# Performance work log

Measured on AMD Instinct MI355X. Metric: run time of the kernel, lower is better.

Reference implementation:

```python
import math
import jax, jax.numpy as jnp
import numpy as np

D_MODEL = 1024
NUM_HEADS = 16
HEAD_DIM = D_MODEL // NUM_HEADS
MAX_REL = 128


def setup_inputs() -> dict:
    key = jax.random.key(0)
    ks = jax.random.split(key, 7)
    B, S = 2, 2048
    s = 1.0 / math.sqrt(D_MODEL)
    return {
        "x": jax.random.normal(ks[0], (B, S, D_MODEL), dtype=jnp.float32),
        "mask": jnp.ones((B, S, S), dtype=jnp.int32),
        "w_q": jax.random.normal(ks[1], (D_MODEL, D_MODEL), dtype=jnp.float32) * s,
        "w_k": jax.random.normal(ks[2], (D_MODEL, D_MODEL), dtype=jnp.float32) * s,
        "w_v": jax.random.normal(ks[3], (D_MODEL, D_MODEL), dtype=jnp.float32) * s,
        "w_o_w": jax.random.normal(ks[4], (D_MODEL, D_MODEL), dtype=jnp.float32) * s,
        "w_o_b": jnp.zeros((D_MODEL,), dtype=jnp.float32),
        "rel_emb": jax.random.normal(ks[5], (2 * MAX_REL + 1, HEAD_DIM), dtype=jnp.float32),
    }


def reference(x, mask, w_q, w_k, w_v, w_o_w, w_o_b, rel_emb):
    B, S, D = x.shape
    H, hd = NUM_HEADS, HEAD_DIM
    scale = math.sqrt(hd)

    def proj(w):  # torch Linear: x @ w.T  -> [B,H,S,hd]
        return (x @ w.T).reshape(B, S, H, hd).transpose(0, 2, 1, 3)

    Q, K, V = proj(w_q), proj(w_k), proj(w_v)

    # content scores (scaled)
    scores = jnp.einsum("bhqd,bhkd->bhqk", Q, K) / scale

    # T5-style relative position bias (NOT scaled, matching source)
    pos = jnp.arange(S)
    dist = jnp.clip(pos[None, :] - pos[:, None], -MAX_REL, MAX_REL) + MAX_REL  # [S,S]
    rel = rel_emb[dist]  # [S,S,hd]
    scores = scores + jnp.einsum("bhqd,qkd->bhqk", Q, rel)

    scores = jnp.where(mask[:, None, :, :] == 0, -1e9, scores)
    attn = jax.nn.softmax(scores, axis=-1)  # [B,H,S,S]

    ctx = jnp.einsum("bhqk,bhkd->bhqd", attn, V)
    ctx = ctx.transpose(0, 2, 1, 3).reshape(B, S, D)
    out = ctx @ w_o_w.T + w_o_b
    return out, attn
```

## Files before the change

### kernel.cpp

```cpp
#include <hip/hip_runtime.h>
#include <hip/hip_bf16.h>

#define B_ 2
#define S_ 2048
#define H_ 16
#define HD_ 64
#define D_ 1024
#define NJ_ 257
#define RSTRIDE_ 264

typedef __bf16 v8bf __attribute__((ext_vector_type(8)));
typedef __bf16 v4bf __attribute__((ext_vector_type(4)));
typedef float  v4f  __attribute__((ext_vector_type(4)));

static __device__ __forceinline__ v4f mfma16(v8bf a, v8bf b, v4f c) {
    return __builtin_amdgcn_mfma_f32_16x16x32_bf16(a, b, c, 0, 0, 0);
}

__global__ void k_split2(const float* __restrict__ src, __bf16* __restrict__ h,
                         __bf16* __restrict__ l, int n4) {
    int i = blockIdx.x * blockDim.x + threadIdx.x;
    int stride = gridDim.x * blockDim.x;
    for (; i < n4; i += stride) {
        const float4 v = ((const float4*)src)[i];
        float vv[4] = {v.x, v.y, v.z, v.w};
        v4bf hv, lv;
#pragma unroll
        for (int j = 0; j < 4; j++) {
            __bf16 hb = (__bf16)vv[j];
            hv[j] = hb;
            lv[j] = (__bf16)(vv[j] - (float)hb);
        }
        *(v4bf*)(h + 4 * (size_t)i) = hv;
        *(v4bf*)(l + 4 * (size_t)i) = lv;
    }
}

__global__ void k_rowflag(const int* __restrict__ mask, unsigned char* __restrict__ flags) {
    const int row = blockIdx.x;
    const int4* mp = (const int4*)(mask + (size_t)row * S_);
    int ok = 1;
    for (int i = threadIdx.x; i < S_ / 4; i += blockDim.x) {
        int4 m = mp[i];
        ok &= (m.x != 0) & (m.y != 0) & (m.z != 0) & (m.w != 0);
    }
    int all = __syncthreads_and(ok);
    if (threadIdx.x == 0) flags[row] = (unsigned char)(all != 0);
}

__global__ __launch_bounds__(256) void k_proj(const __bf16* __restrict__ Ah,
                                              const __bf16* __restrict__ Al,
                                              const __bf16* __restrict__ Bh,
                                              const __bf16* __restrict__ Bl,
                                              __bf16* __restrict__ Oh,
                                              __bf16* __restrict__ Ol) {
    __shared__ __bf16 sAh[64][72], sAl[64][72], sBh[64][72], sBl[64][72];
    const int n0 = blockIdx.x * 64;
    const int m0 = blockIdx.y * 64;
    const int tid = threadIdx.x, lane = tid & 63, wid = tid >> 6;
    const int fr = lane & 15, fo = (lane >> 4) * 8;
    const int srow = tid >> 2, scol = (tid & 3) * 16;
    v4f acc[4] = {};
    for (int k0 = 0; k0 < D_; k0 += 64) {
        const size_t ga = (size_t)(m0 + srow) * D_ + k0 + scol;
        const size_t gb = (size_t)(n0 + srow) * D_ + k0 + scol;
        *(v8bf*)&sAh[srow][scol]     = *(const v8bf*)(Ah + ga);
        *(v8bf*)&sAh[srow][scol + 8] = *(const v8bf*)(Ah + ga + 8);
        *(v8bf*)&sAl[srow][scol]     = *(const v8bf*)(Al + ga);
        *(v8bf*)&sAl[srow][scol + 8] = *(const v8bf*)(Al + ga + 8);
        *(v8bf*)&sBh[srow][scol]     = *(const v8bf*)(Bh + gb);
        *(v8bf*)&sBh[srow][scol + 8] = *(const v8bf*)(Bh + gb + 8);
        *(v8bf*)&sBl[srow][scol]     = *(const v8bf*)(Bl + gb);
        *(v8bf*)&sBl[srow][scol + 8] = *(const v8bf*)(Bl + gb + 8);
        __syncthreads();
#pragma unroll
        for (int ks = 0; ks < 2; ks++) {
            v8bf ah = *(const v8bf*)&sAh[wid * 16 + fr][ks * 32 + fo];
            v8bf al = *(const v8bf*)&sAl[wid * 16 + fr][ks * 32 + fo];
#pragma unroll
            for (int nt = 0; nt < 4; nt++) {
                v8bf bh = *(const v8bf*)&sBh[nt * 16 + fr][ks * 32 + fo];
                v8bf bl = *(const v8bf*)&sBl[nt * 16 + fr][ks * 32 + fo];
                acc[nt] = mfma16(ah, bh, acc[nt]);
                acc[nt] = mfma16(ah, bl, acc[nt]);
                acc[nt] = mfma16(al, bh, acc[nt]);
            }
        }
        __syncthreads();
    }
#pragma unroll
    for (int nt = 0; nt < 4; nt++) {
#pragma unroll
        for (int r = 0; r < 4; r++) {
            const int row = m0 + wid * 16 + (lane >> 4) * 4 + r;
            const int col = n0 + nt * 16 + fr;
            const size_t idx = (size_t)row * D_ + col;
            float f = acc[nt][r];
            __bf16 hb = (__bf16)f;
            Oh[idx] = hb;
            Ol[idx] = (__bf16)(f - (float)hb);
        }
    }
}

__global__ __launch_bounds__(256) void k_projV(const __bf16* __restrict__ A,
                                               const __bf16* __restrict__ Bw,
                                               __bf16* __restrict__ O) {
    __shared__ __bf16 sA[64][72], sB[64][72];
    const int n0 = blockIdx.x * 64;
    const int m0 = blockIdx.y * 64;
    const int tid = threadIdx.x, lane = tid & 63, wid = tid >> 6;
    const int fr = lane & 15, fo = (lane >> 4) * 8;
    const int srow = tid >> 2, scol = (tid & 3) * 16;
    v4f acc[4] = {};
    for (int k0 = 0; k0 < D_; k0 += 64) {
        const size_t ga = (size_t)(m0 + srow) * D_ + k0 + scol;
        const size_t gb = (size_t)(n0 + srow) * D_ + k0 + scol;
        *(v8bf*)&sA[srow][scol]     = *(const v8bf*)(A + ga);
        *(v8bf*)&sA[srow][scol + 8] = *(const v8bf*)(A + ga + 8);
        *(v8bf*)&sB[srow][scol]     = *(const v8bf*)(Bw + gb);
        *(v8bf*)&sB[srow][scol + 8] = *(const v8bf*)(Bw + gb + 8);
        __syncthreads();
#pragma unroll
        for (int ks = 0; ks < 2; ks++) {
            v8bf a = *(const v8bf*)&sA[wid * 16 + fr][ks * 32 + fo];
#pragma unroll
            for (int nt = 0; nt < 4; nt++) {
                v8bf bb = *(const v8bf*)&sB[nt * 16 + fr][ks * 32 + fo];
                acc[nt] = mfma16(a, bb, acc[nt]);
            }
        }
        __syncthreads();
    }
#pragma unroll
    for (int nt = 0; nt < 4; nt++) {
#pragma unroll
        for (int r = 0; r < 4; r++) {
            const int row = m0 + wid * 16 + (lane >> 4) * 4 + r;
            O[(size_t)row * D_ + n0 + nt * 16 + fr] = (__bf16)acc[nt][r];
        }
    }
}

__global__ __launch_bounds__(256) void k_vtrans(const __bf16* __restrict__ Vb,
                                                __bf16* __restrict__ Vt) {
    __shared__ __bf16 t[64][72];
    const int s0 = blockIdx.x * 64, n0 = blockIdx.y * 64, b = blockIdx.z;
    const int tid = threadIdx.x;
    const int r = tid >> 2, c = (tid & 3) * 16;
    const size_t gin = ((size_t)(b * S_ + s0 + r)) * D_ + n0 + c;
    *(v8bf*)&t[r][c]     = *(const v8bf*)(Vb + gin);
    *(v8bf*)&t[r][c + 8] = *(const v8bf*)(Vb + gin + 8);
    __syncthreads();
    v8bf o0, o1;
#pragma unroll
    for (int j = 0; j < 8; j++) { o0[j] = t[c + j][r]; o1[j] = t[c + 8 + j][r]; }
    const size_t gout = ((size_t)(b * D_ + n0 + r)) * S_ + s0 + c;
    *(v8bf*)(Vt + gout)     = o0;
    *(v8bf*)(Vt + gout + 8) = o1;
}

__global__ __launch_bounds__(256) void k_relgemm(const __bf16* __restrict__ Qh,
                                                 const __bf16* __restrict__ Ql,
                                                 const __bf16* __restrict__ relh,
                                                 const __bf16* __restrict__ rell,
                                                 float* __restrict__ Rg) {
    const int q0 = blockIdx.x * 64;
    const int bh = blockIdx.y;
    const int b = bh >> 4, h = bh & 15;
    const int tid = threadIdx.x, lane = tid & 63, wid = tid >> 6;
    const int fr = lane & 15, fo = (lane >> 4) * 8;
    const size_t qbase = (size_t)(b * S_ + q0 + wid * 16 + fr) * D_ + h * HD_;
    v8bf qa_h[2], qa_l[2];
#pragma unroll
    for (int ks = 0; ks < 2; ks++) {
        qa_h[ks] = *(const v8bf*)(Qh + qbase + ks * 32 + fo);
        qa_l[ks] = *(const v8bf*)(Ql + qbase + ks * 32 + fo);
    }
    v4f acc[17] = {};
#pragma unroll
    for (int jt = 0; jt < 17; jt++) {
        int j = jt * 16 + fr;
        if (j > 256) j = 256;
        const size_t rb = (size_t)j * HD_;
#pragma unroll
        for (int ks = 0; ks < 2; ks++) {
            v8bf bh_ = *(const v8bf*)(relh + rb + ks * 32 + fo);
            v8bf bl_ = *(const v8bf*)(rell + rb + ks * 32 + fo);
            acc[jt] = mfma16(qa_h[ks], bh_, acc[jt]);
            acc[jt] = mfma16(qa_h[ks], bl_, acc[jt]);
            acc[jt] = mfma16(qa_l[ks], bh_, acc[jt]);
        }
    }
    const size_t rowbase = ((size_t)bh * S_ + q0 + wid * 16 + (lane >> 4) * 4) * RSTRIDE_;
#pragma unroll
    for (int jt = 0; jt < 17; jt++) {
        const int j = jt * 16 + fr;
        if (j <= 256) {
#pragma unroll
            for (int r = 0; r < 4; r++)
                Rg[rowbase + (size_t)r * RSTRIDE_ + j] = acc[jt][r];
        }
    }
}

__global__ __launch_bounds__(512, 4) void k_stats(const __bf16* __restrict__ Qh,
                                                  const __bf16* __restrict__ Ql,
                                                  const __bf16* __restrict__ Kh,
                                                  const float* __restrict__ Rg,
                                                  const int* __restrict__ mask,
                                                  const unsigned char* __restrict__ flags,
                                                  float* __restrict__ mrow,
                                                  float* __restrict__ lrow) {
    __shared__ __bf16 sK[2][64][72];
    const int flat = blockIdx.x;
    const int swz = (flat & 7) * 64 + (flat >> 3);
    const int qt = swz & 15, bh = swz >> 4;
    const int b = bh >> 4, h = bh & 15;
    const int q0 = qt * 128;
    const int tid = threadIdx.x, lane = tid & 63, w = tid >> 6;
    const int fr = lane & 15, fq = lane >> 4, fo = fq * 8;
    const int myrow = w * 16 + fq * 4;
    const int srow = tid >> 3, sc8 = (tid & 7) * 8;

    const size_t qbase = (size_t)(b * S_ + q0 + w * 16 + fr) * D_ + h * HD_;
    v8bf qa_h[2], qa_l[2];
#pragma unroll
    for (int ks = 0; ks < 2; ks++) {
        qa_h[ks] = *(const v8bf*)(Qh + qbase + ks * 32 + fo);
        qa_l[ks] = *(const v8bf*)(Ql + qbase + ks * 32 + fo);
    }

    const int qg0 = q0 + myrow;
    const size_t rbase0 = ((size_t)bh * S_ + qg0) * RSTRIDE_;
    const size_t mbase0 = ((size_t)b * S_ + qg0) * S_;
    float rcL[4], rcR[4];
    int flr[4];
#pragma unroll
    for (int r = 0; r < 4; r++) {
        rcL[r] = Rg[rbase0 + (size_t)r * RSTRIDE_];
        rcR[r] = Rg[rbase0 + (size_t)r * RSTRIDE_ + 256];
        flr[r] = flags[(size_t)b * S_ + qg0 + r];
    }

    const __bf16* kgbase = Kh + (size_t)(b * S_ + srow) * D_ + h * HD_ + sc8;
    v8bf rk = *(const v8bf*)(kgbase);
    *(v8bf*)&sK[0][srow][sc8] = rk;
    rk = *(const v8bf*)(kgbase + (size_t)64 * D_);
    __syncthreads();

    float mrun[4], lrun[4];
#pragma unroll
    for (int r = 0; r < 4; r++) { mrun[r] = -3.0e38f; lrun[r] = 0.0f; }

    int cur = 0;
    for (int kc = 0; kc < 32; kc++) {
        const int k0 = kc * 64;
        v4f acc[4] = {};
#pragma unroll
        for (int ct = 0; ct < 4; ct++) {
#pragma unroll
            for (int ks = 0; ks < 2; ks++) {
                v8bf kb = *(const v8bf*)&sK[cur][ct * 16 + fr][ks * 32 + fo];
                acc[ct] = mfma16(qa_h[ks], kb, acc[ct]);
                acc[ct] = mfma16(qa_l[ks], kb, acc[ct]);
            }
        }
        const bool band = (kc >= 2 * qt - 3) && (kc <= 2 * qt + 3);
        const bool left = kc < 2 * qt;
#pragma unroll
        for (int r = 0; r < 4; r++) {
            const int qg = qg0 + r;
            float s[4];
#pragma unroll
            for (int ct = 0; ct < 4; ct++) {
                const int k = k0 + ct * 16 + fr;
                float bias;
                if (band) {
                    const int dd = k - qg;
                    const int j = dd < -128 ? 0 : (dd > 128 ? 256 : dd + 128);
                    bias = Rg[rbase0 + (size_t)r * RSTRIDE_ + j];
                } else {
                    bias = left ? rcL[r] : rcR[r];
                }
                float sv = acc[ct][r] * 0.125f + bias;
                if (!flr[r] && mask[mbase0 + (size_t)r * S_ + k] == 0) sv = -1e9f;
                s[ct] = sv;
            }
            const float cm = fmaxf(fmaxf(s[0], s[1]), fmaxf(s[2], s[3]));
            if (cm > mrun[r]) {
                lrun[r] *= __expf(mrun[r] - cm);
                mrun[r] = cm;
            }
            lrun[r] += __expf(s[0] - mrun[r]) + __expf(s[1] - mrun[r]) +
                       __expf(s[2] - mrun[r]) + __expf(s[3] - mrun[r]);
        }
        if (kc < 31) *(v8bf*)&sK[cur ^ 1][srow][sc8] = rk;
        if (kc < 30) rk = *(const v8bf*)(kgbase + (size_t)(k0 + 128) * D_);
        __syncthreads();
        cur ^= 1;
    }

#pragma unroll
    for (int r = 0; r < 4; r++) {
#pragma unroll
        for (int sh = 1; sh < 16; sh <<= 1) {
            const float om = __shfl_xor(mrun[r], sh);
            const float ol = __shfl_xor(lrun[r], sh);
            const float mn = fmaxf(mrun[r], om);
            lrun[r] = lrun[r] * __expf(mrun[r] - mn) + ol * __expf(om - mn);
            mrun[r] = mn;
        }
    }
    if (fr == 0) {
#pragma unroll
        for (int r = 0; r < 4; r++) {
            mrow[(size_t)bh * S_ + qg0 + r] = mrun[r];
            lrow[(size_t)bh * S_ + qg0 + r] = lrun[r];
        }
    }
}

__global__ __launch_bounds__(512, 4) void k_final(const __bf16* __restrict__ Qh,
                                                  const __bf16* __restrict__ Ql,
                                                  const __bf16* __restrict__ Kh,
                                                  const __bf16* __restrict__ Vt,
                                                  const float* __restrict__ Rg,
                                                  const int* __restrict__ mask,
                                                  const unsigned char* __restrict__ flags,
                                                  const float* __restrict__ mrow,
                                                  const float* __restrict__ lrow,
                                                  float* __restrict__ attn,
                                                  __bf16* __restrict__ ctx) {
    __shared__ __bf16 sK[2][64][72], sV[2][64][72], sP[128][72];
    const int flat = blockIdx.x;
    const int swz = (flat & 7) * 64 + (flat >> 3);
    const int qt = swz & 15, bh = swz >> 4;
    const int b = bh >> 4, h = bh & 15;
    const int q0 = qt * 128;
    const int tid = threadIdx.x, lane = tid & 63, w = tid >> 6;
    const int fr = lane & 15, fq = lane >> 4, fo = fq * 8;
    const int myrow = w * 16 + fq * 4;
    const int srow = tid >> 3, sc8 = (tid & 7) * 8;

    const size_t qbase = (size_t)(b * S_ + q0 + w * 16 + fr) * D_ + h * HD_;
    v8bf qa_h[2], qa_l[2];
#pragma unroll
    for (int ks = 0; ks < 2; ks++) {
        qa_h[ks] = *(const v8bf*)(Qh + qbase + ks * 32 + fo);
        qa_l[ks] = *(const v8bf*)(Ql + qbase + ks * 32 + fo);
    }

    const int qg0 = q0 + myrow;
    const size_t rbase0 = ((size_t)bh * S_ + qg0) * RSTRIDE_;
    const size_t mbase0 = ((size_t)b * S_ + qg0) * S_;
    const size_t abase0 = ((size_t)bh * S_ + qg0) * S_;
    float rcL[4], rcR[4], mfin[4], lfin[4];
    int flr[4];
#pragma unroll
    for (int r = 0; r < 4; r++) {
        rcL[r] = Rg[rbase0 + (size_t)r * RSTRIDE_];
        rcR[r] = Rg[rbase0 + (size_t)r * RSTRIDE_ + 256];
        flr[r] = flags[(size_t)b * S_ + qg0 + r];
        mfin[r] = mrow[(size_t)bh * S_ + qg0 + r];
        lfin[r] = 1.0f / lrow[(size_t)bh * S_ + qg0 + r];
    }

    const __bf16* kgbase = Kh + (size_t)(b * S_ + srow) * D_ + h * HD_ + sc8;
    const __bf16* vgbase = Vt + (size_t)(b * D_ + h * HD_ + srow) * S_ + sc8;
    v8bf rk = *(const v8bf*)(kgbase);
    v8bf rv = *(const v8bf*)(vgbase);
    *(v8bf*)&sK[0][srow][sc8] = rk;
    *(v8bf*)&sV[0][srow][sc8] = rv;
    rk = *(const v8bf*)(kgbase + (size_t)64 * D_);
    rv = *(const v8bf*)(vgbase + 64);
    __syncthreads();

    v4f acc2[4] = {};
    int cur = 0;
    for (int kc = 0; kc < 32; kc++) {
        const int k0 = kc * 64;
        v4f acc[4] = {};
#pragma unroll
        for (int ct = 0; ct < 4; ct++) {
#pragma unroll
            for (int ks = 0; ks < 2; ks++) {
                v8bf kb = *(const v8bf*)&sK[cur][ct * 16 + fr][ks * 32 + fo];
                acc[ct] = mfma16(qa_h[ks], kb, acc[ct]);
                acc[ct] = mfma16(qa_l[ks], kb, acc[ct]);
            }
        }
        const bool band = (kc >= 2 * qt - 3) && (kc <= 2 * qt + 3);
        const bool left = kc < 2 * qt;
#pragma unroll
        for (int r = 0; r < 4; r++) {
            const int qg = qg0 + r;
#pragma unroll
            for (int ct = 0; ct < 4; ct++) {
                const int k = k0 + ct * 16 + fr;
                float bias;
                if (band) {
                    const int dd = k - qg;
                    const int j = dd < -128 ? 0 : (dd > 128 ? 256 : dd + 128);
                    bias = Rg[rbase0 + (size_t)r * RSTRIDE_ + j];
                } else {
                    bias = left ? rcL[r] : rcR[r];
                }
                float sv = acc[ct][r] * 0.125f + bias;
                if (!flr[r] && mask[mbase0 + (size_t)r * S_ + k] == 0) sv = -1e9f;
                const float p = __expf(sv - mfin[r]) * lfin[r];
                attn[abase0 + (size_t)r * S_ + k] = p;
                sP[myrow + r][ct * 16 + fr] = (__bf16)p;
            }
        }
        __syncthreads();
#pragma unroll
        for (int ks = 0; ks < 2; ks++) {
            v8bf pa = *(const v8bf*)&sP[w * 16 + fr][ks * 32 + fo];
#pragma unroll
            for (int ct = 0; ct < 4; ct++) {
                v8bf vb = *(const v8bf*)&sV[cur][ct * 16 + fr][ks * 32 + fo];
                acc2[ct] = mfma16(pa, vb, acc2[ct]);
            }
        }
        if (kc < 31) {
            *(v8bf*)&sK[cur ^ 1][srow][sc8] = rk;
            *(v8bf*)&sV[cur ^ 1][srow][sc8] = rv;
        }
        if (kc < 30) {
            rk = *(const v8bf*)(kgbase + (size_t)(k0 + 128) * D_);
            rv = *(const v8bf*)(vgbase + k0 + 128);
        }
        __syncthreads();
        cur ^= 1;
    }

#pragma unroll
    for (int ct = 0; ct < 4; ct++) {
#pragma unroll
        for (int r = 0; r < 4; r++) {
            const int qg = qg0 + r;
            const int d = ct * 16 + fr;
            ctx[(size_t)(b * S_ + qg) * D_ + h * HD_ + d] = (__bf16)acc2[ct][r];
        }
    }
}

__global__ __launch_bounds__(256) void k_outproj(const __bf16* __restrict__ A,
                                                 const __bf16* __restrict__ Bw,
                                                 const float* __restrict__ bias,
                                                 float* __restrict__ out) {
    __shared__ __bf16 sA[64][72], sB[64][72];
    const int n0 = blockIdx.x * 64;
    const int m0 = blockIdx.y * 64;
    const int tid = threadIdx.x, lane = tid & 63, wid = tid >> 6;
    const int fr = lane & 15, fo = (lane >> 4) * 8;
    const int srow = tid >> 2, scol = (tid & 3) * 16;
    v4f acc[4] = {};
    for (int k0 = 0; k0 < D_; k0 += 64) {
        const size_t ga = (size_t)(m0 + srow) * D_ + k0 + scol;
        const size_t gb = (size_t)(n0 + srow) * D_ + k0 + scol;
        *(v8bf*)&sA[srow][scol]     = *(const v8bf*)(A + ga);
        *(v8bf*)&sA[srow][scol + 8] = *(const v8bf*)(A + ga + 8);
        *(v8bf*)&sB[srow][scol]     = *(const v8bf*)(Bw + gb);
        *(v8bf*)&sB[srow][scol + 8] = *(const v8bf*)(Bw + gb + 8);
        __syncthreads();
#pragma unroll
        for (int ks = 0; ks < 2; ks++) {
            v8bf a = *(const v8bf*)&sA[wid * 16 + fr][ks * 32 + fo];
#pragma unroll
            for (int nt = 0; nt < 4; nt++) {
                v8bf bb = *(const v8bf*)&sB[nt * 16 + fr][ks * 32 + fo];
                acc[nt] = mfma16(a, bb, acc[nt]);
            }
        }
        __syncthreads();
    }
#pragma unroll
    for (int nt = 0; nt < 4; nt++) {
        const float bv = bias[n0 + nt * 16 + fr];
#pragma unroll
        for (int r = 0; r < 4; r++) {
            const int row = m0 + wid * 16 + (lane >> 4) * 4 + r;
            out[(size_t)row * D_ + n0 + nt * 16 + fr] = acc[nt][r] + bv;
        }
    }
}

extern "C" void kernel_launch(void* const* d_in, const int* in_sizes, int n_in,
                              void* d_out, int out_size, void* d_ws, size_t ws_size,
                              hipStream_t stream) {
    (void)in_sizes; (void)n_in; (void)out_size; (void)ws_size;
    const float* x    = (const float*)d_in[0];
    const int*   mask = (const int*)d_in[1];
    const float* wq   = (const float*)d_in[2];
    const float* wk   = (const float*)d_in[3];
    const float* wv   = (const float*)d_in[4];
    const float* wo   = (const float*)d_in[5];
    const float* wob  = (const float*)d_in[6];
    const float* rel  = (const float*)d_in[7];
    float* out  = (float*)d_out;
    float* attn = out + (size_t)B_ * S_ * D_;

    char* p = (char*)d_ws;
    auto alloc = [&](size_t bytes) -> char* {
        char* r = p;
        p += (bytes + 255) & ~(size_t)255;
        return r;
    };
    const size_t BSD = (size_t)B_ * S_ * D_;
    const size_t DD  = (size_t)D_ * D_;
    __bf16* xh   = (__bf16*)alloc(BSD * 2);
    __bf16* xl   = (__bf16*)alloc(BSD * 2);
    __bf16* wqh  = (__bf16*)alloc(DD * 2);
    __bf16* wql  = (__bf16*)alloc(DD * 2);
    __bf16* wkh  = (__bf16*)alloc(DD * 2);
    __bf16* wkl  = (__bf16*)alloc(DD * 2);
    __bf16* wvh  = (__bf16*)alloc(DD * 2);
    __bf16* wvl  = (__bf16*)alloc(DD * 2);
    __bf16* woh  = (__bf16*)alloc(DD * 2);
    __bf16* wol  = (__bf16*)alloc(DD * 2);
    __bf16* relh = (__bf16*)alloc((size_t)NJ_ * HD_ * 2);
    __bf16* rell = (__bf16*)alloc((size_t)NJ_ * HD_ * 2);
    __bf16* Qh   = (__bf16*)alloc(BSD * 2);
    __bf16* Ql   = (__bf16*)alloc(BSD * 2);
    __bf16* Kh   = (__bf16*)alloc(BSD * 2);
    __bf16* Kl   = (__bf16*)alloc(BSD * 2);
    __bf16* Vb   = (__bf16*)alloc(BSD * 2);
    __bf16* Vt   = (__bf16*)alloc(BSD * 2);
    float*  Rg   = (float*)alloc((size_t)B_ * H_ * S_ * RSTRIDE_ * 4);
    float*  mrow = (float*)alloc((size_t)B_ * H_ * S_ * 4);
    float*  lrow = (float*)alloc((size_t)B_ * H_ * S_ * 4);
    __bf16* ctx  = (__bf16*)alloc(BSD * 2);
    unsigned char* flags = (unsigned char*)alloc((size_t)B_ * S_);

    k_split2<<<2048, 256, 0, stream>>>(x, xh, xl, (int)(BSD / 4));
    k_split2<<<1024, 256, 0, stream>>>(wq, wqh, wql, (int)(DD / 4));
    k_split2<<<1024, 256, 0, stream>>>(wk, wkh, wkl, (int)(DD / 4));
    k_split2<<<1024, 256, 0, stream>>>(wv, wvh, wvl, (int)(DD / 4));
    k_split2<<<1024, 256, 0, stream>>>(wo, woh, wol, (int)(DD / 4));
    k_split2<<<17, 256, 0, stream>>>(rel, relh, rell, (int)(NJ_ * HD_ / 4));

    k_rowflag<<<B_ * S_, 256, 0, stream>>>(mask, flags);

    k_proj<<<dim3(D_ / 64, B_ * S_ / 64), 256, 0, stream>>>(xh, xl, wqh, wql, Qh, Ql);
    k_proj<<<dim3(D_ / 64, B_ * S_ / 64), 256, 0, stream>>>(xh, xl, wkh, wkl, Kh, Kl);
    k_projV<<<dim3(D_ / 64, B_ * S_ / 64), 256, 0, stream>>>(xh, wvh, Vb);

    k_vtrans<<<dim3(S_ / 64, D_ / 64, B_), 256, 0, stream>>>(Vb, Vt);

    k_relgemm<<<dim3(S_ / 64, B_ * H_), 256, 0, stream>>>(Qh, Ql, relh, rell, Rg);

    k_stats<<<512, 512, 0, stream>>>(Qh, Ql, Kh, Rg, mask, flags, mrow, lrow);

    k_final<<<512, 512, 0, stream>>>(Qh, Ql, Kh, Vt, Rg, mask, flags, mrow, lrow, attn, ctx);

    k_outproj<<<dim3(D_ / 64, B_ * S_ / 64), 256, 0, stream>>>(ctx, woh, wob, out);
}
```

Before: 608.9 us.

## Fuse stats and final attention passes into one kernel with direct global K/V reads

Merges the row-statistics kernel and the final probability/context kernel into one kernel that runs two passes over K per block, so the mrow/lrow intermediates and one launch are no longer needed. It also drops the shared-memory double-buffered K/V staging and block-wide barriers. Each wave now reads K and V fragments straight from global memory and keeps its P tile in a per-wave shared slice. This removes synchronisation and LDS traffic but relies on cache for K/V reuse across the 8 waves, which may raise global memory traffic and load latency.

```diff
diff --git a/kernel.cpp b/kernel.cpp
--- a/kernel.cpp
+++ b/kernel.cpp
@@ -204,15 +204,16 @@
     }
 }
 
-__global__ __launch_bounds__(512, 4) void k_stats(const __bf16* __restrict__ Qh,
+__global__ __launch_bounds__(512, 4) void k_attn2(const __bf16* __restrict__ Qh,
                                                   const __bf16* __restrict__ Ql,
                                                   const __bf16* __restrict__ Kh,
+                                                  const __bf16* __restrict__ Vt,
                                                   const float* __restrict__ Rg,
                                                   const int* __restrict__ mask,
                                                   const unsigned char* __restrict__ flags,
-                                                  float* __restrict__ mrow,
-                                                  float* __restrict__ lrow) {
-    __shared__ __bf16 sK[2][64][72];
+                                                  float* __restrict__ attn,
+                                                  __bf16* __restrict__ ctx) {
+    __shared__ __bf16 sP[8][16][72];
     const int flat = blockIdx.x;
     const int swz = (flat & 7) * 64 + (flat >> 3);
     const int qt = swz & 15, bh = swz >> 4;
@@ -220,8 +221,7 @@
     const int q0 = qt * 128;
     const int tid = threadIdx.x, lane = tid & 63, w = tid >> 6;
     const int fr = lane & 15, fq = lane >> 4, fo = fq * 8;
-    const int myrow = w * 16 + fq * 4;
-    const int srow = tid >> 3, sc8 = (tid & 7) * 8;
+    const int qg0 = q0 + w * 16 + fq * 4;
 
     const size_t qbase = (size_t)(b * S_ + q0 + w * 16 + fr) * D_ + h * HD_;
     v8bf qa_h[2], qa_l[2];
@@ -231,9 +231,9 @@
         qa_l[ks] = *(const v8bf*)(Ql + qbase + ks * 32 + fo);
     }
 
-    const int qg0 = q0 + myrow;
     const size_t rbase0 = ((size_t)bh * S_ + qg0) * RSTRIDE_;
     const size_t mbase0 = ((size_t)b * S_ + qg0) * S_;
+    const size_t abase0 = ((size_t)bh * S_ + qg0) * S_;
     float rcL[4], rcR[4];
     int flr[4];
 #pragma unroll
@@ -243,28 +243,25 @@
         flr[r] = flags[(size_t)b * S_ + qg0 + r];
     }
 
-    const __bf16* kgbase = Kh + (size_t)(b * S_ + srow) * D_ + h * HD_ + sc8;
-    v8bf rk = *(const v8bf*)(kgbase);
-    *(v8bf*)&sK[0][srow][sc8] = rk;
-    rk = *(const v8bf*)(kgbase + (size_t)64 * D_);
-    __syncthreads();
+    const __bf16* kpanel = Kh + (size_t)b * S_ * D_ + h * HD_;
+    const __bf16* vpanel = Vt + (size_t)(b * D_ + h * HD_) * S_;
 
     float mrun[4], lrun[4];
 #pragma unroll
     for (int r = 0; r < 4; r++) { mrun[r] = -3.0e38f; lrun[r] = 0.0f; }
 
-    int cur = 0;
     for (int kc = 0; kc < 32; kc++) {
         const int k0 = kc * 64;
         v4f acc[4] = {};
 #pragma unroll
         for (int ct = 0; ct < 4; ct++) {
-#pragma unroll
-            for (int ks = 0; ks < 2; ks++) {
-                v8bf kb = *(const v8bf*)&sK[cur][ct * 16 + fr][ks * 32 + fo];
-                acc[ct] = mfma16(qa_h[ks], kb, acc[ct]);
-                acc[ct] = mfma16(qa_l[ks], kb, acc[ct]);
-            }
+            const size_t krow = (size_t)(k0 + ct * 16 + fr) * D_;
+            v8bf kb0 = *(const v8bf*)(kpanel + krow + fo);
+            v8bf kb1 = *(const v8bf*)(kpanel + krow + 32 + fo);
+            acc[ct] = mfma16(qa_h[0], kb0, acc[ct]);
+            acc[ct] = mfma16(qa_l[0], kb0, acc[ct]);
+            acc[ct] = mfma16(qa_h[1], kb1, acc[ct]);
+            acc[ct] = mfma16(qa_l[1], kb1, acc[ct]);
         }
         const bool band = (kc >= 2 * qt - 3) && (kc <= 2 * qt + 3);
         const bool left = kc < 2 * qt;
@@ -295,12 +292,9 @@
             lrun[r] += __expf(s[0] - mrun[r]) + __expf(s[1] - mrun[r]) +
                        __expf(s[2] - mrun[r]) + __expf(s[3] - mrun[r]);
         }
-        if (kc < 31) *(v8bf*)&sK[cur ^ 1][srow][sc8] = rk;
-        if (kc < 30) rk = *(const v8bf*)(kgbase + (size_t)(k0 + 128) * D_);
-        __syncthreads();
-        cur ^= 1;
-    }
-
+    }
+
+    float mfin[4], lfin[4];
 #pragma unroll
     for (int r = 0; r < 4; r++) {
 #pragma unroll
@@ -311,84 +305,23 @@
             lrun[r] = lrun[r] * __expf(mrun[r] - mn) + ol * __expf(om - mn);
             mrun[r] = mn;
         }
-    }
-    if (fr == 0) {
-#pragma unroll
-        for (int r = 0; r < 4; r++) {
-            mrow[(size_t)bh * S_ + qg0 + r] = mrun[r];
-            lrow[(size_t)bh * S_ + qg0 + r] = lrun[r];
-        }
-    }
-}
-
-__global__ __launch_bounds__(512, 4) void k_final(const __bf16* __restrict__ Qh,
-                                                  const __bf16* __restrict__ Ql,
-                                                  const __bf16* __restrict__ Kh,
-                                                  const __bf16* __restrict__ Vt,
-                                                  const float* __restrict__ Rg,
-                                                  const int* __restrict__ mask,
-                                                  const unsigned char* __restrict__ flags,
-                                                  const float* __restrict__ mrow,
-                                                  const float* __restrict__ lrow,
-                                                  float* __restrict__ attn,
-                                                  __bf16* __restrict__ ctx) {
-    __shared__ __bf16 sK[2][64][72], sV[2][64][72], sP[128][72];
-    const int flat = blockIdx.x;
-    const int swz = (flat & 7) * 64 + (flat >> 3);
-    const int qt = swz & 15, bh = swz >> 4;
-    const int b = bh >> 4, h = bh & 15;
-    const int q0 = qt * 128;
-    const int tid = threadIdx.x, lane = tid & 63, w = tid >> 6;
-    const int fr = lane & 15, fq = lane >> 4, fo = fq * 8;
-    const int myrow = w * 16 + fq * 4;
-    const int srow = tid >> 3, sc8 = (tid & 7) * 8;
-
-    const size_t qbase = (size_t)(b * S_ + q0 + w * 16 + fr) * D_ + h * HD_;
-    v8bf qa_h[2], qa_l[2];
-#pragma unroll
-    for (int ks = 0; ks < 2; ks++) {
-        qa_h[ks] = *(const v8bf*)(Qh + qbase + ks * 32 + fo);
-        qa_l[ks] = *(const v8bf*)(Ql + qbase + ks * 32 + fo);
-    }
-
-    const int qg0 = q0 + myrow;
-    const size_t rbase0 = ((size_t)bh * S_ + qg0) * RSTRIDE_;
-    const size_t mbase0 = ((size_t)b * S_ + qg0) * S_;
-    const size_t abase0 = ((size_t)bh * S_ + qg0) * S_;
-    float rcL[4], rcR[4], mfin[4], lfin[4];
-    int flr[4];
-#pragma unroll
-    for (int r = 0; r < 4; r++) {
-        rcL[r] = Rg[rbase0 + (size_t)r * RSTRIDE_];
-        rcR[r] = Rg[rbase0 + (size_t)r * RSTRIDE_ + 256];
-        flr[r] = flags[(size_t)b * S_ + qg0 + r];
-        mfin[r] = mrow[(size_t)bh * S_ + qg0 + r];
-        lfin[r] = 1.0f / lrow[(size_t)bh * S_ + qg0 + r];
-    }
-
-    const __bf16* kgbase = Kh + (size_t)(b * S_ + srow) * D_ + h * HD_ + sc8;
-    const __bf16* vgbase = Vt + (size_t)(b * D_ + h * HD_ + srow) * S_ + sc8;
-    v8bf rk = *(const v8bf*)(kgbase);
-    v8bf rv = *(const v8bf*)(vgbase);
-    *(v8bf*)&sK[0][srow][sc8] = rk;
-    *(v8bf*)&sV[0][srow][sc8] = rv;
-    rk = *(const v8bf*)(kgbase + (size_t)64 * D_);
-    rv = *(const v8bf*)(vgbase + 64);
-    __syncthreads();
+        mfin[r] = mrun[r];
+        lfin[r] = 1.0f / lrun[r];
+    }
 
     v4f acc2[4] = {};
-    int cur = 0;
     for (int kc = 0; kc < 32; kc++) {
         const int k0 = kc * 64;
         v4f acc[4] = {};
 #pragma unroll
         for (int ct = 0; ct < 4; ct++) {
-#pragma unroll
-            for (int ks = 0; ks < 2; ks++) {
-                v8bf kb = *(const v8bf*)&sK[cur][ct * 16 + fr][ks * 32 + fo];
-                acc[ct] = mfma16(qa_h[ks], kb, acc[ct]);
-                acc[ct] = mfma16(qa_l[ks], kb, acc[ct]);
-            }
+            const size_t krow = (size_t)(k0 + ct * 16 + fr) * D_;
+            v8bf kb0 = *(const v8bf*)(kpanel + krow + fo);
+            v8bf kb1 = *(const v8bf*)(kpanel + krow + 32 + fo);
+            acc[ct] = mfma16(qa_h[0], kb0, acc[ct]);
+            acc[ct] = mfma16(qa_l[0], kb0, acc[ct]);
+            acc[ct] = mfma16(qa_h[1], kb1, acc[ct]);
+            acc[ct] = mfma16(qa_l[1], kb1, acc[ct]);
         }
         const bool band = (kc >= 2 * qt - 3) && (kc <= 2 * qt + 3);
         const bool left = kc < 2 * qt;
@@ -410,29 +343,19 @@
                 if (!flr[r] && mask[mbase0 + (size_t)r * S_ + k] == 0) sv = -1e9f;
                 const float p = __expf(sv - mfin[r]) * lfin[r];
                 attn[abase0 + (size_t)r * S_ + k] = p;
-                sP[myrow + r][ct * 16 + fr] = (__bf16)p;
-            }
-        }
-        __syncthreads();
+                sP[w][fq * 4 + r][ct * 16 + fr] = (__bf16)p;
+            }
+        }
 #pragma unroll
         for (int ks = 0; ks < 2; ks++) {
-            v8bf pa = *(const v8bf*)&sP[w * 16 + fr][ks * 32 + fo];
+            v8bf pa = *(const v8bf*)&sP[w][fr][ks * 32 + fo];
 #pragma unroll
             for (int ct = 0; ct < 4; ct++) {
-                v8bf vb = *(const v8bf*)&sV[cur][ct * 16 + fr][ks * 32 + fo];
+                const size_t vrow = (size_t)(ct * 16 + fr) * S_;
+                v8bf vb = *(const v8bf*)(vpanel + vrow + k0 + ks * 32 + fo);
                 acc2[ct] = mfma16(pa, vb, acc2[ct]);
             }
         }
-        if (kc < 31) {
-            *(v8bf*)&sK[cur ^ 1][srow][sc8] = rk;
-            *(v8bf*)&sV[cur ^ 1][srow][sc8] = rv;
-        }
-        if (kc < 30) {
-            rk = *(const v8bf*)(kgbase + (size_t)(k0 + 128) * D_);
-            rv = *(const v8bf*)(vgbase + k0 + 128);
-        }
-        __syncthreads();
-        cur ^= 1;
     }
 
 #pragma unroll
@@ -529,8 +452,6 @@
     __bf16* Vb   = (__bf16*)alloc(BSD * 2);
     __bf16* Vt   = (__bf16*)alloc(BSD * 2);
     float*  Rg   = (float*)alloc((size_t)B_ * H_ * S_ * RSTRIDE_ * 4);
-    float*  mrow = (float*)alloc((size_t)B_ * H_ * S_ * 4);
-    float*  lrow = (float*)alloc((size_t)B_ * H_ * S_ * 4);
     __bf16* ctx  = (__bf16*)alloc(BSD * 2);
     unsigned char* flags = (unsigned char*)alloc((size_t)B_ * S_);
 
@@ -551,9 +472,7 @@
 
     k_relgemm<<<dim3(S_ / 64, B_ * H_), 256, 0, stream>>>(Qh, Ql, relh, rell, Rg);
 
-    k_stats<<<512, 512, 0, stream>>>(Qh, Ql, Kh, Rg, mask, flags, mrow, lrow);
-
-    k_final<<<512, 512, 0, stream>>>(Qh, Ql, Kh, Vt, Rg, mask, flags, mrow, lrow, attn, ctx);
+    k_attn2<<<512, 512, 0, stream>>>(Qh, Ql, Kh, Vt, Rg, mask, flags, attn, ctx);
 
     k_outproj<<<dim3(D_ / 64, B_ * S_ / 64), 256, 0, stream>>>(ctx, woh, wob, out);
 }
```

Result: slower. 765.8 us (+25.8%).
